# Kernel tuning notes

Measured on AMD Instinct MI355X. Metric: run time of the kernel, lower is better.

## Reference

```python
import jax, jax.numpy as jnp
import numpy as np

N_HEAD = 12
N_EMBD = 768
HEAD_DIM = N_EMBD // N_HEAD


def setup_inputs() -> dict:
    key = jax.random.key(0)
    k1, k2, k3, k4, k5 = jax.random.split(key, 5)
    B, T, C = 1, 4096, N_EMBD
    s = 0.02
    return {
        "x": jax.random.normal(k1, (B, T, C), dtype=jnp.float32),
        "W_qkv": jax.random.normal(k2, (C, 3 * C), dtype=jnp.float32) * s,
        "b_qkv": jnp.zeros((3 * C,), dtype=jnp.float32),
        "W_out": jax.random.normal(k3, (C, C), dtype=jnp.float32) * s,
        "b_out": jnp.zeros((C,), dtype=jnp.float32),
    }


def reference(x, W_qkv, b_qkv, W_out, b_out):
    B, T, C = x.shape
    H, D = N_HEAD, HEAD_DIM
    qkv = x @ W_qkv + b_qkv                       # (B, T, 3C)
    qkv = qkv.reshape(B, T, 3, H, D)
    q = jnp.transpose(qkv[:, :, 0], (0, 2, 1, 3))  # (B, H, T, D)
    k = jnp.transpose(qkv[:, :, 1], (0, 2, 1, 3))
    v = jnp.transpose(qkv[:, :, 2], (0, 2, 1, 3))
    scores = jnp.einsum("bhqd,bhkd->bhqk", q, k) / jnp.sqrt(jnp.float32(D))
    causal = jnp.tril(jnp.ones((T, T), dtype=bool))
    scores = jnp.where(causal[None, None], scores, -jnp.inf)
    weights = jax.nn.softmax(scores, axis=-1)     # (B, H, T, T)
    out = jnp.einsum("bhqk,bhkd->bhqd", weights, v)
    out = jnp.transpose(out, (0, 2, 1, 3)).reshape(B, T, C)
    return out @ W_out + b_out
```

## Files before the change

### kernel.cpp

```cpp
#include <hip/hip_runtime.h>
#include <hip/hip_bf16.h>
#include <stdint.h>

#define T_SEQ 4096
#define C_EMB 768
#define C3    2304
#define CQK   1536
#define NH    12
#define HD    64
#define CH    16
#define NSLOT 1728

typedef __attribute__((ext_vector_type(8))) short short8;
typedef __attribute__((ext_vector_type(4))) short short4v;
typedef __attribute__((ext_vector_type(4))) float f32x4;

__device__ __forceinline__ short f2bf(float f) {
  __bf16 h = (__bf16)f;
  return __builtin_bit_cast(short, h);
}

__device__ __forceinline__ void gload_lds16(const void* g, void* l) {
  __builtin_amdgcn_global_load_lds((const __attribute__((address_space(1))) void*)g,
                                   (__attribute__((address_space(3))) void*)l, 16, 0, 0);
}

__global__ __launch_bounds__(256)
void cvt_kernel(const float* __restrict__ in, short* __restrict__ out, int n4) {
  int i = blockIdx.x * 256 + threadIdx.x;
  if (i < n4) {
    float4 v = ((const float4*)in)[i];
    short4v s = { f2bf(v.x), f2bf(v.y), f2bf(v.z), f2bf(v.w) };
    ((short4v*)out)[i] = s;
  }
}

__global__ __launch_bounds__(256)
void transpose_cvt_kernel(const float* __restrict__ W, short* __restrict__ WT,
                          int K, int N) {
  __shared__ float ts[32][33];
  const int r0 = blockIdx.y * 32, c0 = blockIdx.x * 32;
  const int tid = threadIdx.x;
  {
    int rr = tid >> 3, c4 = (tid & 7) * 4;
    float4 v = *(const float4*)(W + (size_t)(r0 + rr) * N + c0 + c4);
    ts[rr][c4 + 0] = v.x; ts[rr][c4 + 1] = v.y;
    ts[rr][c4 + 2] = v.z; ts[rr][c4 + 3] = v.w;
  }
  __syncthreads();
  {
    int nr = tid >> 3, k4 = (tid & 7) * 4;
    short4v s = { f2bf(ts[k4 + 0][nr]), f2bf(ts[k4 + 1][nr]),
                  f2bf(ts[k4 + 2][nr]), f2bf(ts[k4 + 3][nr]) };
    *(short4v*)(WT + (size_t)(c0 + nr) * K + r0 + k4) = s;
  }
}

template<int BN, bool SPLIT_V, bool OUT_F32>
__global__ __launch_bounds__(256)
void gemm_kernel(const short* __restrict__ A, const short* __restrict__ Bt,
                 const float* __restrict__ bias, void* __restrict__ Cp,
                 short* __restrict__ Kfp, short* __restrict__ Vfp,
                 int N, int K) {
  constexpr int MF = (BN == 128) ? 4 : 2;
  __shared__ short As[128 * 32];
  __shared__ short Bs[BN * 32];
  const int row0 = blockIdx.y * 128, col0 = blockIdx.x * BN;
  const int tid = threadIdx.x, lane = tid & 63, wave = tid >> 6;
  const int lg = lane >> 4, lr = lane & 15;
  const int wr = (BN == 128) ? ((wave >> 1) * 64) : (wave * 32);
  const int wc = (BN == 128) ? ((wave & 1) * 64) : 0;

  f32x4 acc[MF][4];
  #pragma unroll
  for (int m_ = 0; m_ < MF; ++m_)
    #pragma unroll
    for (int n_ = 0; n_ < 4; ++n_) acc[m_][n_] = (f32x4){0.f, 0.f, 0.f, 0.f};

  const int srow = wave * 16 + (lane >> 2);
  const int scol = (lane & 3) * 8;

  for (int kt = 0; kt < K; kt += 32) {
    __syncthreads();
    #pragma unroll
    for (int c = 0; c < 2; ++c)
      gload_lds16(A + (size_t)(row0 + c * 64 + srow) * K + kt + scol,
                  As + c * 2048 + wave * 512);
    #pragma unroll
    for (int c = 0; c < BN / 64; ++c)
      gload_lds16(Bt + (size_t)(col0 + c * 64 + srow) * K + kt + scol,
                  Bs + c * 2048 + wave * 512);
    __syncthreads();

    short8 a[MF], b[4];
    #pragma unroll
    for (int m_ = 0; m_ < MF; ++m_)
      a[m_] = *(const short8*)&As[(wr + m_ * 16 + lr) * 32 + lg * 8];
    #pragma unroll
    for (int n_ = 0; n_ < 4; ++n_)
      b[n_] = *(const short8*)&Bs[(wc + n_ * 16 + lr) * 32 + lg * 8];
    #pragma unroll
    for (int m_ = 0; m_ < MF; ++m_)
      #pragma unroll
      for (int n_ = 0; n_ < 4; ++n_)
        acc[m_][n_] = __builtin_amdgcn_mfma_f32_16x16x32_bf16(a[m_], b[n_], acc[m_][n_], 0, 0, 0);
  }

  const bool isK = SPLIT_V && (col0 >= C_EMB) && (col0 < CQK);
  const bool isV = SPLIT_V && (col0 >= CQK);
  #pragma unroll
  for (int n_ = 0; n_ < 4; ++n_) {
    const int col = col0 + wc + n_ * 16 + lr;
    const float bv = bias[col];
    #pragma unroll
    for (int m_ = 0; m_ < MF; ++m_) {
      const int rbase = row0 + wr + m_ * 16 + lg * 4;
      if constexpr (OUT_F32) {
        #pragma unroll
        for (int r = 0; r < 4; ++r)
          ((float*)Cp)[(size_t)(rbase + r) * N + col] = acc[m_][n_][r] + bv;
      } else if constexpr (!SPLIT_V) {
        #pragma unroll
        for (int r = 0; r < 4; ++r)
          ((short*)Cp)[(size_t)(rbase + r) * N + col] = f2bf(acc[m_][n_][r] + bv);
      } else {
        if (!isV) {
          const int fcol = col & 63;
          const int hh = (col >> 6) - (isK ? (C_EMB >> 6) : 0);
          const int ks = (fcol >> 5) & 1, lgf = (fcol >> 3) & 3, e = fcol & 7;
          const int tile = rbase >> 6, pair = (rbase >> 4) & 3, lrt = rbase & 15;
          short* base = isK ? Kfp : (short*)Cp;
          const size_t idx =
              ((((size_t)(hh * 64 + tile) * 8 + pair * 2 + ks) * 64) +
               lgf * 16 + lrt) * 8 + e;
          #pragma unroll
          for (int r = 0; r < 4; ++r)
            base[idx + r * 8] = f2bf(acc[m_][n_][r] + bv);
        } else {
          const int dv = col - CQK;
          const int hh = dv >> 6, fv = dv & 63, dd = fv >> 4, lrv = fv & 15;
          const int t64 = rbase & 63;
          const int p64 = (t64 & 32) + ((t64 & 12) << 1) + ((t64 & 16) >> 2);
          const int kt2 = rbase >> 6;
          short4v pck = { f2bf(acc[m_][n_][0] + bv), f2bf(acc[m_][n_][1] + bv),
                          f2bf(acc[m_][n_][2] + bv), f2bf(acc[m_][n_][3] + bv) };
          const size_t idx =
              ((((size_t)(hh * 64 + kt2) * 8 + dd * 2 + (p64 >> 5)) * 64) +
               ((p64 >> 3) & 3) * 16 + lrv) * 8 + (p64 & 7);
          *(short4v*)(Vfp + idx) = pck;
        }
      }
    }
  }
}

__global__ __launch_bounds__(256, 3)
void attn_kernel(const short* __restrict__ Qf, const short* __restrict__ Kf,
                 const short* __restrict__ Vf, short* __restrict__ out,
                 float* __restrict__ pO, float* __restrict__ pML) {
  const int jj = blockIdx.x * 4 + (threadIdx.x >> 6);
  const int lane = threadIdx.x & 63;
  const int pr = jj >> 1, qh = jj & 1;
  const int h = pr % NH;
  const int ii = 159 - pr / NH;
  int qt, ck;
  if (ii < 16)      { qt = ii;                 ck = 0; }
  else if (ii < 48) { qt = 16 + (ii - 16) / 2; ck = (ii - 16) % 2; }
  else if (ii < 96) { qt = 32 + (ii - 48) / 3; ck = (ii - 48) % 3; }
  else              { qt = 48 + (ii - 96) / 4; ck = (ii - 96) % 4; }
  const int q0 = qt * 64;
  const int ntiles = qt + 1;
  const int t0 = ck * CH;
  const int rem = ntiles - t0;
  const int nloc = rem < CH ? rem : CH;

  const int lg = lane >> 4, lr = lane & 15;
  const float SC = 0.18033688011f;

  const short* Qb = Qf + ((size_t)(h * 64 + qt) * 8) * 512 + lane * 8;
  short8 qfr[2][2];
  #pragma unroll
  for (int g = 0; g < 2; ++g)
    #pragma unroll
    for (int ks = 0; ks < 2; ++ks)
      qfr[g][ks] = *(const short8*)(Qb + ((qh * 2 + g) * 2 + ks) * 512);

  float mrun[2] = { -1e30f, -1e30f }, lrun[2] = { 0.f, 0.f };
  f32x4 o[4][2];
  #pragma unroll
  for (int d = 0; d < 4; ++d)
    #pragma unroll
    for (int g = 0; g < 2; ++g) o[d][g] = (f32x4){0.f, 0.f, 0.f, 0.f};

  const short* Kp = Kf + ((size_t)(h * 64 + t0) * 8) * 512 + lane * 8;
  const short* Vp = Vf + ((size_t)(h * 64 + t0) * 8) * 512 + lane * 8;

  for (int tt = 0; tt < nloc; ++tt) {
    const int tl = t0 + tt;

    short8 kf_[4][2], vf_[4][2];
    #pragma unroll
    for (int n = 0; n < 4; ++n)
      #pragma unroll
      for (int ks = 0; ks < 2; ++ks)
        kf_[n][ks] = *(const short8*)(Kp + (n * 2 + ks) * 512);
    #pragma unroll
    for (int d = 0; d < 4; ++d)
      #pragma unroll
      for (int ks = 0; ks < 2; ++ks)
        vf_[d][ks] = *(const short8*)(Vp + (d * 2 + ks) * 512);
    Kp += 4096;
    Vp += 4096;

    #pragma unroll
    for (int g = 0; g < 2; ++g) {
      f32x4 s[4];
      __builtin_amdgcn_s_setprio(1);
      #pragma unroll
      for (int n = 0; n < 4; ++n) {
        f32x4 cc = (f32x4){0.f, 0.f, 0.f, 0.f};
        #pragma unroll
        for (int ks = 0; ks < 2; ++ks)
          cc = __builtin_amdgcn_mfma_f32_16x16x32_bf16(kf_[n][ks], qfr[g][ks], cc, 0, 0, 0);
        s[n] = cc;
      }
      __builtin_amdgcn_s_setprio(0);

      if (tl == ntiles - 1) {
        #pragma unroll
        for (int n = 0; n < 4; ++n)
          #pragma unroll
          for (int r = 0; r < 4; ++r)
            if (n * 16 + lg * 4 + r > qh * 32 + g * 16 + lr) s[n][r] = -1e30f;
      }

      float pmax = s[0][0];
      #pragma unroll
      for (int n = 0; n < 4; ++n)
        #pragma unroll
        for (int r = 0; r < 4; ++r) pmax = fmaxf(pmax, s[n][r]);
      pmax = fmaxf(pmax, __shfl_xor(pmax, 16));
      pmax = fmaxf(pmax, __shfl_xor(pmax, 32));

      if (!__all(pmax <= mrun[g] + 44.0f)) {
        const float mn = fmaxf(mrun[g], pmax);
        const float al = exp2f((mrun[g] - mn) * SC);
        lrun[g] *= al;
        #pragma unroll
        for (int d = 0; d < 4; ++d) o[d][g] *= al;
        mrun[g] = mn;
      }
      const float msc = mrun[g] * SC;

      float psum = 0.f;
      #pragma unroll
      for (int n = 0; n < 4; ++n)
        #pragma unroll
        for (int r = 0; r < 4; ++r) {
          float p = exp2f(fmaf(s[n][r], SC, -msc));
          s[n][r] = p;
          psum += p;
        }
      psum += __shfl_xor(psum, 16);
      psum += __shfl_xor(psum, 32);
      lrun[g] += psum;

      __builtin_amdgcn_s_setprio(1);
      #pragma unroll
      for (int ks = 0; ks < 2; ++ks) {
        short8 pb = { f2bf(s[2 * ks][0]),     f2bf(s[2 * ks][1]),
                      f2bf(s[2 * ks][2]),     f2bf(s[2 * ks][3]),
                      f2bf(s[2 * ks + 1][0]), f2bf(s[2 * ks + 1][1]),
                      f2bf(s[2 * ks + 1][2]), f2bf(s[2 * ks + 1][3]) };
        #pragma unroll
        for (int d = 0; d < 4; ++d)
          o[d][g] = __builtin_amdgcn_mfma_f32_16x16x32_bf16(vf_[d][ks], pb, o[d][g], 0, 0, 0);
      }
      __builtin_amdgcn_s_setprio(0);
    }
  }

  if (qt < CH) {
    #pragma unroll
    for (int g = 0; g < 2; ++g) {
      const float linv = 1.f / lrun[g];
      const size_t qrow = q0 + qh * 32 + g * 16 + lr;
      #pragma unroll
      for (int d = 0; d < 4; ++d) {
        short4v ov;
        #pragma unroll
        for (int r = 0; r < 4; ++r) ov[r] = f2bf(o[d][g][r] * linv);
        *(short4v*)(out + qrow * C_EMB + h * HD + d * 16 + lg * 4) = ov;
      }
    }
  } else {
    const int sbase = (qt < 32) ? 2 * (qt - 16)
                    : (qt < 48) ? 32 + 3 * (qt - 32)
                                : 80 + 4 * (qt - 48);
    const int slot = h * 144 + sbase + ck;
    #pragma unroll
    for (int g = 0; g < 2; ++g) {
      const int row = qh * 32 + g * 16 + lr;
      float* po = pO + (size_t)slot * 4096 + row * 64;
      #pragma unroll
      for (int d = 0; d < 4; ++d)
        *(f32x4*)&po[d * 16 + lg * 4] = o[d][g];
      if (lg == 0) {
        pML[(size_t)slot * 128 + row * 2 + 0] = mrun[g];
        pML[(size_t)slot * 128 + row * 2 + 1] = lrun[g];
      }
    }
  }
}

__global__ __launch_bounds__(256)
void merge_kernel(const float* __restrict__ pO, const float* __restrict__ pML,
                  short* __restrict__ out) {
  const int bd = blockIdx.x;
  const int h = bd % NH;
  const int qt = 16 + bd / NH;
  const int nc = qt / CH + 1;
  const int sbase = (qt < 32) ? 2 * (qt - 16)
                  : (qt < 48) ? 32 + 3 * (qt - 32)
                              : 80 + 4 * (qt - 48);
  const int slot0 = h * 144 + sbase;
  const int tid = threadIdx.x;
  const int q = tid >> 2, dc = (tid & 3) << 4;
  const float SC = 0.18033688011f;

  float mi[4], li[4];
  float M = -1e30f;
  #pragma unroll
  for (int i = 0; i < 4; ++i)
    if (i < nc) {
      mi[i] = pML[(size_t)(slot0 + i) * 128 + q * 2 + 0];
      li[i] = pML[(size_t)(slot0 + i) * 128 + q * 2 + 1];
      M = fmaxf(M, mi[i]);
    }

  f32x4 O[4];
  #pragma unroll
  for (int d4 = 0; d4 < 4; ++d4) O[d4] = (f32x4){0.f, 0.f, 0.f, 0.f};
  float L = 0.f;
  #pragma unroll
  for (int i = 0; i < 4; ++i)
    if (i < nc) {
      const float a = exp2f((mi[i] - M) * SC);
      L = fmaf(li[i], a, L);
      const float* po = pO + (size_t)(slot0 + i) * 4096 + q * 64 + dc;
      #pragma unroll
      for (int d4 = 0; d4 < 4; ++d4) {
        f32x4 v = *(const f32x4*)(po + d4 * 4);
        #pragma unroll
        for (int r = 0; r < 4; ++r) O[d4][r] = fmaf(v[r], a, O[d4][r]);
      }
    }

  const float linv = 1.f / L;
  #pragma unroll
  for (int d4 = 0; d4 < 4; ++d4) {
    short4v ov;
    #pragma unroll
    for (int r = 0; r < 4; ++r) ov[r] = f2bf(O[d4][r] * linv);
    *(short4v*)(out + (size_t)(qt * 64 + q) * C_EMB + h * HD + dc + d4 * 4) = ov;
  }
}

extern "C" void kernel_launch(void* const* d_in, const int* in_sizes, int n_in,
                              void* d_out, int out_size, void* d_ws, size_t ws_size,
                              hipStream_t stream) {
  const float* x    = (const float*)d_in[0];
  const float* Wqkv = (const float*)d_in[1];
  const float* bqkv = (const float*)d_in[2];
  const float* Wout = (const float*)d_in[3];
  const float* bout = (const float*)d_in[4];

  short* xb    = (short*)d_ws;
  short* WqkvT = xb    + (size_t)T_SEQ * C_EMB;
  short* WoutT = WqkvT + (size_t)C3 * C_EMB;
  short* Qf    = WoutT + (size_t)C_EMB * C_EMB;
  short* Kf    = Qf    + (size_t)T_SEQ * C_EMB;
  short* Vf    = Kf    + (size_t)T_SEQ * C_EMB;
  float* pO    = (float*)(Vf + (size_t)T_SEQ * C_EMB);
  float* pML   = pO + (size_t)NSLOT * 4096;

  cvt_kernel<<<(T_SEQ * C_EMB / 4) / 256, 256, 0, stream>>>(x, xb, T_SEQ * C_EMB / 4);
  transpose_cvt_kernel<<<dim3(C3 / 32, C_EMB / 32), 256, 0, stream>>>(Wqkv, WqkvT, C_EMB, C3);
  transpose_cvt_kernel<<<dim3(C_EMB / 32, C_EMB / 32), 256, 0, stream>>>(Wout, WoutT, C_EMB, C_EMB);

  gemm_kernel<128, true, false><<<dim3(C3 / 128, T_SEQ / 128), 256, 0, stream>>>(
      xb, WqkvT, bqkv, Qf, Kf, Vf, C3, C_EMB);

  attn_kernel<<<dim3(960), 256, 0, stream>>>(Qf, Kf, Vf, xb, pO, pML);
  merge_kernel<<<dim3(NH * 48), 256, 0, stream>>>(pO, pML, xb);

  gemm_kernel<64, false, true><<<dim3(C_EMB / 64, T_SEQ / 128), 256, 0, stream>>>(
      xb, WoutT, bout, d_out, nullptr, nullptr, C_EMB, C_EMB);
}
```

Measured before the change: 130.2 us.

## Split attention work to one 16-row query group per wave with XCD-aware block mapping

Each wave now handles a single 16-row query group instead of two, so a block of four waves covers one 64-row query tile. The grid doubles to 1920 blocks, and jobs are remapped so that all blocks on an XCD work on the same head, which improves K/V L2 reuse. Register pressure drops, so launch bounds rise to 4 blocks per SIMD for occupancy. The cost is that K/V fragments are now loaded once per 16 query rows instead of once per 32, doubling global/L2 traffic per unit of work.

Result: slower. 136.6 us (+4.9%).

```diff
diff --git a/kernel.cpp b/kernel.cpp
--- a/kernel.cpp
+++ b/kernel.cpp
@@ -154,15 +154,16 @@
   }
 }
 
-__global__ __launch_bounds__(256, 3)
+__global__ __launch_bounds__(256, 4)
 void attn_kernel(const short* __restrict__ Qf, const short* __restrict__ Kf,
                  const short* __restrict__ Vf, short* __restrict__ out,
                  float* __restrict__ pO, float* __restrict__ pML) {
-  const int jj = blockIdx.x * 4 + (threadIdx.x >> 6);
   const int lane = threadIdx.x & 63;
-  const int pr = jj >> 1, qh = jj & 1;
-  const int h = pr % NH;
-  const int ii = 159 - pr / NH;
+  const int qq = threadIdx.x >> 6;
+  const int xcd = blockIdx.x & 7, within = blockIdx.x >> 3;
+  const int job = xcd * 240 + within;
+  const int h = job / 160;
+  const int ii = 159 - (job % 160);
   int qt, ck;
   if (ii < 16)      { qt = ii;                 ck = 0; }
   else if (ii < 48) { qt = 16 + (ii - 16) / 2; ck = (ii - 16) % 2; }
@@ -178,19 +179,15 @@
   const float SC = 0.18033688011f;
 
   const short* Qb = Qf + ((size_t)(h * 64 + qt) * 8) * 512 + lane * 8;
-  short8 qfr[2][2];
-  #pragma unroll
-  for (int g = 0; g < 2; ++g)
-    #pragma unroll
-    for (int ks = 0; ks < 2; ++ks)
-      qfr[g][ks] = *(const short8*)(Qb + ((qh * 2 + g) * 2 + ks) * 512);
-
-  float mrun[2] = { -1e30f, -1e30f }, lrun[2] = { 0.f, 0.f };
-  f32x4 o[4][2];
-  #pragma unroll
-  for (int d = 0; d < 4; ++d)
-    #pragma unroll
-    for (int g = 0; g < 2; ++g) o[d][g] = (f32x4){0.f, 0.f, 0.f, 0.f};
+  short8 qfr[2];
+  #pragma unroll
+  for (int ks = 0; ks < 2; ++ks)
+    qfr[ks] = *(const short8*)(Qb + (qq * 2 + ks) * 512);
+
+  float mrun = -1e30f, lrun = 0.f;
+  f32x4 o[4];
+  #pragma unroll
+  for (int d = 0; d < 4; ++d) o[d] = (f32x4){0.f, 0.f, 0.f, 0.f};
 
   const short* Kp = Kf + ((size_t)(h * 64 + t0) * 8) * 512 + lane * 8;
   const short* Vp = Vf + ((size_t)(h * 64 + t0) * 8) * 512 + lane * 8;
@@ -212,103 +209,94 @@
     Kp += 4096;
     Vp += 4096;
 
-    #pragma unroll
-    for (int g = 0; g < 2; ++g) {
-      f32x4 s[4];
-      __builtin_amdgcn_s_setprio(1);
-      #pragma unroll
-      for (int n = 0; n < 4; ++n) {
-        f32x4 cc = (f32x4){0.f, 0.f, 0.f, 0.f};
-        #pragma unroll
-        for (int ks = 0; ks < 2; ++ks)
-          cc = __builtin_amdgcn_mfma_f32_16x16x32_bf16(kf_[n][ks], qfr[g][ks], cc, 0, 0, 0);
-        s[n] = cc;
-      }
-      __builtin_amdgcn_s_setprio(0);
-
-      if (tl == ntiles - 1) {
-        #pragma unroll
-        for (int n = 0; n < 4; ++n)
-          #pragma unroll
-          for (int r = 0; r < 4; ++r)
-            if (n * 16 + lg * 4 + r > qh * 32 + g * 16 + lr) s[n][r] = -1e30f;
-      }
-
-      float pmax = s[0][0];
+    f32x4 s[4];
+    __builtin_amdgcn_s_setprio(1);
+    #pragma unroll
+    for (int n = 0; n < 4; ++n) {
+      f32x4 cc = (f32x4){0.f, 0.f, 0.f, 0.f};
+      #pragma unroll
+      for (int ks = 0; ks < 2; ++ks)
+        cc = __builtin_amdgcn_mfma_f32_16x16x32_bf16(kf_[n][ks], qfr[ks], cc, 0, 0, 0);
+      s[n] = cc;
+    }
+    __builtin_amdgcn_s_setprio(0);
+
+    if (tl == ntiles - 1) {
       #pragma unroll
       for (int n = 0; n < 4; ++n)
         #pragma unroll
-        for (int r = 0; r < 4; ++r) pmax = fmaxf(pmax, s[n][r]);
-      pmax = fmaxf(pmax, __shfl_xor(pmax, 16));
-      pmax = fmaxf(pmax, __shfl_xor(pmax, 32));
-
-      if (!__all(pmax <= mrun[g] + 44.0f)) {
-        const float mn = fmaxf(mrun[g], pmax);
-        const float al = exp2f((mrun[g] - mn) * SC);
-        lrun[g] *= al;
-        #pragma unroll
-        for (int d = 0; d < 4; ++d) o[d][g] *= al;
-        mrun[g] = mn;
+        for (int r = 0; r < 4; ++r)
+          if (n * 16 + lg * 4 + r > qq * 16 + lr) s[n][r] = -1e30f;
+    }
+
+    float pmax = s[0][0];
+    #pragma unroll
+    for (int n = 0; n < 4; ++n)
+      #pragma unroll
+      for (int r = 0; r < 4; ++r) pmax = fmaxf(pmax, s[n][r]);
+    pmax = fmaxf(pmax, __shfl_xor(pmax, 16));
+    pmax = fmaxf(pmax, __shfl_xor(pmax, 32));
+
+    if (!__all(pmax <= mrun + 44.0f)) {
+      const float mn = fmaxf(mrun, pmax);
+      const float al = exp2f((mrun - mn) * SC);
+      lrun *= al;
+      #pragma unroll
+      for (int d = 0; d < 4; ++d) o[d] *= al;
+      mrun = mn;
+    }
+    const float msc = mrun * SC;
+
+    float psum = 0.f;
+    #pragma unroll
+    for (int n = 0; n < 4; ++n)
+      #pragma unroll
+      for (int r = 0; r < 4; ++r) {
+        float p = exp2f(fmaf(s[n][r], SC, -msc));
+        s[n][r] = p;
+        psum += p;
       }
-      const float msc = mrun[g] * SC;
-
-      float psum = 0.f;
-      #pragma unroll
-      for (int n = 0; n < 4; ++n)
-        #pragma unroll
-        for (int r = 0; r < 4; ++r) {
-          float p = exp2f(fmaf(s[n][r], SC, -msc));
-          s[n][r] = p;
-          psum += p;
-        }
-      psum += __shfl_xor(psum, 16);
-      psum += __shfl_xor(psum, 32);
-      lrun[g] += psum;
-
-      __builtin_amdgcn_s_setprio(1);
-      #pragma unroll
-      for (int ks = 0; ks < 2; ++ks) {
-        short8 pb = { f2bf(s[2 * ks][0]),     f2bf(s[2 * ks][1]),
-                      f2bf(s[2 * ks][2]),     f2bf(s[2 * ks][3]),
-                      f2bf(s[2 * ks + 1][0]), f2bf(s[2 * ks + 1][1]),
-                      f2bf(s[2 * ks + 1][2]), f2bf(s[2 * ks + 1][3]) };
-        #pragma unroll
-        for (int d = 0; d < 4; ++d)
-          o[d][g] = __builtin_amdgcn_mfma_f32_16x16x32_bf16(vf_[d][ks], pb, o[d][g], 0, 0, 0);
-      }
-      __builtin_amdgcn_s_setprio(0);
-    }
+    psum += __shfl_xor(psum, 16);
+    psum += __shfl_xor(psum, 32);
+    lrun += psum;
+
+    __builtin_amdgcn_s_setprio(1);
+    #pragma unroll
+    for (int ks = 0; ks < 2; ++ks) {
+      short8 pb = { f2bf(s[2 * ks][0]),     f2bf(s[2 * ks][1]),
+                    f2bf(s[2 * ks][2]),     f2bf(s[2 * ks][3]),
+                    f2bf(s[2 * ks + 1][0]), f2bf(s[2 * ks + 1][1]),
+                    f2bf(s[2 * ks + 1][2]), f2bf(s[2 * ks + 1][3]) };
+      #pragma unroll
+      for (int d = 0; d < 4; ++d)
+        o[d] = __builtin_amdgcn_mfma_f32_16x16x32_bf16(vf_[d][ks], pb, o[d], 0, 0, 0);
+    }
+    __builtin_amdgcn_s_setprio(0);
   }
 
   if (qt < CH) {
-    #pragma unroll
-    for (int g = 0; g < 2; ++g) {
-      const float linv = 1.f / lrun[g];
-      const size_t qrow = q0 + qh * 32 + g * 16 + lr;
-      #pragma unroll
-      for (int d = 0; d < 4; ++d) {
-        short4v ov;
-        #pragma unroll
-        for (int r = 0; r < 4; ++r) ov[r] = f2bf(o[d][g][r] * linv);
-        *(short4v*)(out + qrow * C_EMB + h * HD + d * 16 + lg * 4) = ov;
-      }
+    const float linv = 1.f / lrun;
+    const size_t qrow = q0 + qq * 16 + lr;
+    #pragma unroll
+    for (int d = 0; d < 4; ++d) {
+      short4v ov;
+      #pragma unroll
+      for (int r = 0; r < 4; ++r) ov[r] = f2bf(o[d][r] * linv);
+      *(short4v*)(out + qrow * C_EMB + h * HD + d * 16 + lg * 4) = ov;
     }
   } else {
     const int sbase = (qt < 32) ? 2 * (qt - 16)
                     : (qt < 48) ? 32 + 3 * (qt - 32)
                                 : 80 + 4 * (qt - 48);
     const int slot = h * 144 + sbase + ck;
-    #pragma unroll
-    for (int g = 0; g < 2; ++g) {
-      const int row = qh * 32 + g * 16 + lr;
-      float* po = pO + (size_t)slot * 4096 + row * 64;
-      #pragma unroll
-      for (int d = 0; d < 4; ++d)
-        *(f32x4*)&po[d * 16 + lg * 4] = o[d][g];
-      if (lg == 0) {
-        pML[(size_t)slot * 128 + row * 2 + 0] = mrun[g];
-        pML[(size_t)slot * 128 + row * 2 + 1] = lrun[g];
-      }
+    const int row = qq * 16 + lr;
+    float* po = pO + (size_t)slot * 4096 + row * 64;
+    #pragma unroll
+    for (int d = 0; d < 4; ++d)
+      *(f32x4*)&po[d * 16 + lg * 4] = o[d];
+    if (lg == 0) {
+      pML[(size_t)slot * 128 + row * 2 + 0] = mrun;
+      pML[(size_t)slot * 128 + row * 2 + 1] = lrun;
     }
   }
 }
@@ -391,7 +379,7 @@
   gemm_kernel<128, true, false><<<dim3(C3 / 128, T_SEQ / 128), 256, 0, stream>>>(
       xb, WqkvT, bqkv, Qf, Kf, Vf, C3, C_EMB);
 
-  attn_kernel<<<dim3(960), 256, 0, stream>>>(Qf, Kf, Vf, xb, pO, pML);
+  attn_kernel<<<dim3(1920), 256, 0, stream>>>(Qf, Kf, Vf, xb, pO, pML);
   merge_kernel<<<dim3(NH * 48), 256, 0, stream>>>(pO, pML, xb);
 
   gemm_kernel<64, false, true><<<dim3(C_EMB / 64, T_SEQ / 128), 256, 0, stream>>>(
```
